# Kernel tuning notes

Measured on AMD Instinct MI355X. Metric: run time of the kernel, lower is better.

Reference implementation:

```python
import jax, jax.numpy as jnp
import numpy as np

B, C, H, W = 16, 256, 32, 32
NUM_LAYERS = 30
OUT = 16  # sqrt(out_channels)
EPS = 1e-5


def setup_inputs() -> dict:
    key = jax.random.key(0)
    k1, k2, k3 = jax.random.split(key, 3)
    x = jax.random.normal(k1, (B, C, H, W), dtype=jnp.float32)
    # delta_t ~ small positive values (module inits ~N(0.01, 0.005))
    delta_t = jax.random.uniform(k2, (NUM_LAYERS, 1), dtype=jnp.float32) * 0.02
    matrices = jax.random.normal(k3, (NUM_LAYERS, 1, 1, OUT, OUT), dtype=jnp.float32) * 0.1
    gamma = jnp.ones((H * W,), dtype=jnp.float32)   # BatchNorm2d weight, oc = i*i = H*W
    beta = jnp.zeros((H * W,), dtype=jnp.float32)   # BatchNorm2d bias
    return {"x": x, "delta_t": delta_t, "matrices": matrices, "gamma": gamma, "beta": beta}


def _bn_relu6(z, gamma, beta):
    # training-mode BatchNorm2d over channel axis 1 (channels = H*W), then ReLU6
    mean = jnp.mean(z, axis=(0, 2, 3), keepdims=True)
    var = jnp.mean(jnp.square(z - mean), axis=(0, 2, 3), keepdims=True)  # biased var
    zhat = (z - mean) * jax.lax.rsqrt(var + EPS)
    g = gamma.reshape(1, -1, 1, 1)
    b = beta.reshape(1, -1, 1, 1)
    return jnp.clip(zhat * g + b, 0.0, 6.0)


def reference(x, delta_t, matrices, gamma, beta):
    b, c, h, w = x.shape
    hw = h * w
    # feature_reshape: [B,C,H,W] -> [B,HW,C] -> [B,HW,out,out] (inn == out branch)
    x1 = x.reshape(b, c, hw).transpose(0, 2, 1).reshape(b, hw, OUT, OUT)
    dt = jnp.clip(delta_t, 0.0, 6.0)[:, 0]  # relu6(delta_t), shape [L]

    def step(y0, params):
        m, dtl = params  # m: [1,1,out,out] broadcasts elementwise against x1
        dydt = -y0 + _bn_relu6(y0 + m * x1, gamma, beta)
        return y0 + dtl * dydt, None

    y0, _ = jax.lax.scan(step, x1, (matrices, dt))
    # (y0 + x1): [B, HW, out, out] -> view [B,H,W,out*out] -> permute to [B,out*out,H,W]
    y = (y0 + x1).reshape(b, h, w, OUT * OUT).transpose(0, 3, 1, 2)
    return y
```

## Files before the change

kernel.cpp:

```cpp
#include <hip/hip_runtime.h>

typedef float v2f __attribute__((ext_vector_type(2)));

#define HW      1024
#define BC      4096
#define NLAYERS 30
#define TPB     256

__global__ __launch_bounds__(TPB) void ode_fused(const float* __restrict__ x,
                                                 const float* __restrict__ delta_t,
                                                 const float* __restrict__ matrices,
                                                 const float* __restrict__ gamma,
                                                 const float* __restrict__ beta,
                                                 float* __restrict__ out) {
    const int bid = blockIdx.x;
    const int p   = ((bid & 7) << 7) | (bid >> 3);
    const int t   = threadIdx.x;

    __shared__ float smat[NLAYERS * 256];
    __shared__ float sdt[NLAYERS];
    __shared__ v2f   red[2][4];

#pragma unroll
    for (int i = 0; i < NLAYERS; ++i)
        smat[i * 256 + t] = matrices[i * 256 + t];
    if (t < NLAYERS)
        sdt[t] = __builtin_amdgcn_fmed3f(delta_t[t], 0.0f, 6.0f);

    v2f x1[8], y[8];
#pragma unroll
    for (int k = 0; k < 8; ++k) {
        x1[k].x = x[(size_t)(t + 512 * k) * HW + p];
        x1[k].y = x[(size_t)(t + 512 * k + 256) * HW + p];
        y[k] = x1[k];
    }

    const float gp   = gamma[p];
    const float bp   = beta[p];
    const int   wid  = t >> 6;
    const int   lane = t & 63;

    __syncthreads();

    for (int l = 0; l < NLAYERS; ++l) {
        const float m   = smat[l * 256 + t];
        const float dtl = sdt[l];
        const v2f m2 = {m, m};

        v2f z[8];
        v2f sA = {0.f, 0.f}, sB = {0.f, 0.f};
        v2f qA = {0.f, 0.f}, qB = {0.f, 0.f};
#pragma unroll
        for (int k = 0; k < 8; k += 2) {
            z[k]     = __builtin_elementwise_fma(m2, x1[k], y[k]);
            z[k + 1] = __builtin_elementwise_fma(m2, x1[k + 1], y[k + 1]);
            sA += z[k];
            sB += z[k + 1];
            qA = __builtin_elementwise_fma(z[k], z[k], qA);
            qB = __builtin_elementwise_fma(z[k + 1], z[k + 1], qB);
        }
        const v2f sv = sA + sB;
        const v2f qv = qA + qB;
        v2f pr; pr.x = sv.x + sv.y; pr.y = qv.x + qv.y;

#pragma unroll
        for (int mask = 1; mask < 64; mask <<= 1) {
            v2f o;
            o.x = __shfl_xor(pr.x, mask, 64);
            o.y = __shfl_xor(pr.y, mask, 64);
            pr += o;
        }
        const int par = l & 1;
        if (lane == 0) red[par][wid] = pr;
        __syncthreads();
        const v2f tot = red[par][0] + red[par][1] + red[par][2] + red[par][3];

        const float mean = tot.x * (1.0f / 4096.0f);
        const float var  = fmaf(-mean, mean, tot.y * (1.0f / 4096.0f));
        const float rstd = rsqrtf(var + 1e-5f);
        const float g    = gp * rstd;
        const float bb   = fmaf(-mean, g, bp);
        const v2f g2  = {g, g},   b2 = {bb, bb};
        const v2f dt2 = {dtl, dtl};
        const v2f z2  = {0.f, 0.f}, s6 = {6.f, 6.f};
#pragma unroll
        for (int k = 0; k < 8; ++k) {
            v2f a = __builtin_elementwise_fma(z[k], g2, b2);
            a = __builtin_elementwise_max(a, z2);
            a = __builtin_elementwise_min(a, s6);
            y[k] = __builtin_elementwise_fma(dt2, a - y[k], y[k]);
        }
    }

#pragma unroll
    for (int k = 0; k < 8; ++k) {
        out[(size_t)(t + 512 * k) * HW + p]       = y[k].x + x1[k].x;
        out[(size_t)(t + 512 * k + 256) * HW + p] = y[k].y + x1[k].y;
    }
}

extern "C" void kernel_launch(void* const* d_in, const int* in_sizes, int n_in,
                              void* d_out, int out_size, void* d_ws, size_t ws_size,
                              hipStream_t stream) {
    const float* x        = (const float*)d_in[0];
    const float* delta_t  = (const float*)d_in[1];
    const float* matrices = (const float*)d_in[2];
    const float* gamma    = (const float*)d_in[3];
    const float* beta     = (const float*)d_in[4];
    float* out = (float*)d_out;

    ode_fused<<<dim3(HW), dim3(TPB), 0, stream>>>(x, delta_t, matrices, gamma, beta, out);
}
```

Measured before the change: 121.7 us.

## Process two BN channels per block with float2 I/O and DPP wave reductions

Each block now handles two adjacent spatial channels with 512 threads instead of one channel with 256, so global loads and stores of x and out become 8-byte float2 accesses. The shuffle-xor reduction is replaced by DPP row/broadcast adds, and the next layer's matrix value and dt are prefetched before the barrier. The update is rewritten as y*(1-dt) + dt*clip(...), with clipping done by fmed3. Halving the grid to 512 blocks may reduce occupancy across CUs.

```diff
diff --git a/kernel.cpp b/kernel.cpp
--- a/kernel.cpp
+++ b/kernel.cpp
@@ -3,9 +3,29 @@
 typedef float v2f __attribute__((ext_vector_type(2)));
 
 #define HW      1024
-#define BC      4096
 #define NLAYERS 30
-#define TPB     256
+#define TPB     512
+
+template <int CTRL, int RMASK>
+__device__ __forceinline__ v2f dpp_add2(v2f x) {
+    int a = __builtin_amdgcn_update_dpp(0, __builtin_bit_cast(int, x.x),
+                                        CTRL, RMASK, 0xf, true);
+    int b = __builtin_amdgcn_update_dpp(0, __builtin_bit_cast(int, x.y),
+                                        CTRL, RMASK, 0xf, true);
+    v2f r;
+    r.x = x.x + __builtin_bit_cast(float, a);
+    r.y = x.y + __builtin_bit_cast(float, b);
+    return r;
+}
+__device__ __forceinline__ v2f wave_sum64_v2(v2f x) {
+    x = dpp_add2<0x111, 0xf>(x);
+    x = dpp_add2<0x112, 0xf>(x);
+    x = dpp_add2<0x114, 0xf>(x);
+    x = dpp_add2<0x118, 0xf>(x);
+    x = dpp_add2<0x142, 0xa>(x);
+    x = dpp_add2<0x143, 0xc>(x);
+    return x;
+}
 
 __global__ __launch_bounds__(TPB) void ode_fused(const float* __restrict__ x,
                                                  const float* __restrict__ delta_t,
@@ -13,39 +33,44 @@
                                                  const float* __restrict__ gamma,
                                                  const float* __restrict__ beta,
                                                  float* __restrict__ out) {
-    const int bid = blockIdx.x;
-    const int p   = ((bid & 7) << 7) | (bid >> 3);
-    const int t   = threadIdx.x;
+    const int bid  = blockIdx.x;
+    const int pA   = ((bid & 7) << 7) | ((bid >> 3) << 1);
+    const int t    = threadIdx.x;
+    const int c    = t & 255;
+    const int wid  = t >> 6;
+    const int lane = t & 63;
 
-    __shared__ float smat[NLAYERS * 256];
-    __shared__ float sdt[NLAYERS];
-    __shared__ v2f   red[2][4];
+    __shared__ float smat[(NLAYERS + 1) * 256];
+    __shared__ float sdt[NLAYERS + 1];
+    __shared__ __align__(16) float4 red[2][8];
 
-#pragma unroll
-    for (int i = 0; i < NLAYERS; ++i)
-        smat[i * 256 + t] = matrices[i * 256 + t];
-    if (t < NLAYERS)
-        sdt[t] = __builtin_amdgcn_fmed3f(delta_t[t], 0.0f, 6.0f);
+    for (int i = t; i < NLAYERS * 256; i += TPB)
+        smat[i] = matrices[i];
+    if (t < NLAYERS) sdt[t] = __builtin_amdgcn_fmed3f(delta_t[t], 0.0f, 6.0f);
+    if (t == 0) sdt[NLAYERS] = 0.0f;
 
+    const float2* __restrict__ xp = (const float2*)(x + pA);
     v2f x1[8], y[8];
 #pragma unroll
     for (int k = 0; k < 8; ++k) {
-        x1[k].x = x[(size_t)(t + 512 * k) * HW + p];
-        x1[k].y = x[(size_t)(t + 512 * k + 256) * HW + p];
+        const float2 v = xp[(size_t)(t + 512 * k) * (HW / 2)];
+        x1[k].x = v.x; x1[k].y = v.y;
         y[k] = x1[k];
     }
 
-    const float gp   = gamma[p];
-    const float bp   = beta[p];
-    const int   wid  = t >> 6;
-    const int   lane = t & 63;
+    const float2 gpv = *(const float2*)(gamma + pA);
+    const float2 bpv = *(const float2*)(beta + pA);
+    const v2f gp2 = {gpv.x, gpv.y};
+    const v2f bp2 = {bpv.x, bpv.y};
 
     __syncthreads();
+    float m_cur = smat[c];
+    float dtl   = sdt[0];
 
     for (int l = 0; l < NLAYERS; ++l) {
-        const float m   = smat[l * 256 + t];
-        const float dtl = sdt[l];
-        const v2f m2 = {m, m};
+        const v2f m2  = {m_cur, m_cur};
+        const v2f dt2 = {dtl, dtl};
+        const v2f om2 = {1.0f - dtl, 1.0f - dtl};
 
         v2f z[8];
         v2f sA = {0.f, 0.f}, sB = {0.f, 0.f};
@@ -59,43 +84,52 @@
             qA = __builtin_elementwise_fma(z[k], z[k], qA);
             qB = __builtin_elementwise_fma(z[k + 1], z[k + 1], qB);
         }
-        const v2f sv = sA + sB;
-        const v2f qv = qA + qB;
-        v2f pr; pr.x = sv.x + sv.y; pr.y = qv.x + qv.y;
+#pragma unroll
+        for (int k = 0; k < 8; ++k) y[k] *= om2;
 
+        const v2f sv = wave_sum64_v2(sA + sB);
+        const v2f qv = wave_sum64_v2(qA + qB);
+
+        const int par = l & 1;
+        if (lane == 63) {
+            float4 w; w.x = sv.x; w.y = sv.y; w.z = qv.x; w.w = qv.y;
+            red[par][wid] = w;
+        }
+        m_cur = smat[(l + 1) * 256 + c];
+        const float dtn = sdt[l + 1];
+        __syncthreads();
+
+        float4 acc = red[par][0];
 #pragma unroll
-        for (int mask = 1; mask < 64; mask <<= 1) {
-            v2f o;
-            o.x = __shfl_xor(pr.x, mask, 64);
-            o.y = __shfl_xor(pr.y, mask, 64);
-            pr += o;
+        for (int w = 1; w < 8; ++w) {
+            const float4 r = red[par][w];
+            acc.x += r.x; acc.y += r.y; acc.z += r.z; acc.w += r.w;
         }
-        const int par = l & 1;
-        if (lane == 0) red[par][wid] = pr;
-        __syncthreads();
-        const v2f tot = red[par][0] + red[par][1] + red[par][2] + red[par][3];
+        const v2f S = {acc.x, acc.y};
+        const v2f Q = {acc.z, acc.w};
 
-        const float mean = tot.x * (1.0f / 4096.0f);
-        const float var  = fmaf(-mean, mean, tot.y * (1.0f / 4096.0f));
-        const float rstd = rsqrtf(var + 1e-5f);
-        const float g    = gp * rstd;
-        const float bb   = fmaf(-mean, g, bp);
-        const v2f g2  = {g, g},   b2 = {bb, bb};
-        const v2f dt2 = {dtl, dtl};
-        const v2f z2  = {0.f, 0.f}, s6 = {6.f, 6.f};
+        const v2f mean = S * (1.0f / 4096.0f);
+        v2f var = Q * (1.0f / 4096.0f) - mean * mean;
+        v2f rstd; rstd.x = rsqrtf(var.x + 1e-5f); rstd.y = rsqrtf(var.y + 1e-5f);
+        const v2f g  = gp2 * rstd;
+        const v2f bb = bp2 - mean * g;
 #pragma unroll
         for (int k = 0; k < 8; ++k) {
-            v2f a = __builtin_elementwise_fma(z[k], g2, b2);
-            a = __builtin_elementwise_max(a, z2);
-            a = __builtin_elementwise_min(a, s6);
-            y[k] = __builtin_elementwise_fma(dt2, a - y[k], y[k]);
+            v2f a = __builtin_elementwise_fma(z[k], g, bb);
+            a.x = __builtin_amdgcn_fmed3f(a.x, 0.0f, 6.0f);
+            a.y = __builtin_amdgcn_fmed3f(a.y, 0.0f, 6.0f);
+            y[k] = __builtin_elementwise_fma(dt2, a, y[k]);
         }
+        dtl = dtn;
     }
 
+    float2* __restrict__ outp = (float2*)(out + pA);
 #pragma unroll
     for (int k = 0; k < 8; ++k) {
-        out[(size_t)(t + 512 * k) * HW + p]       = y[k].x + x1[k].x;
-        out[(size_t)(t + 512 * k + 256) * HW + p] = y[k].y + x1[k].y;
+        float2 w;
+        w.x = y[k].x + x1[k].x;
+        w.y = y[k].y + x1[k].y;
+        outp[(size_t)(t + 512 * k) * (HW / 2)] = w;
     }
 }
 
@@ -109,5 +143,6 @@
     const float* beta     = (const float*)d_in[4];
     float* out = (float*)d_out;
 
-    ode_fused<<<dim3(HW), dim3(TPB), 0, stream>>>(x, delta_t, matrices, gamma, beta, out);
+    ode_fused<<<dim3(HW / 2), dim3(TPB), 0, stream>>>(x, delta_t, matrices,
+                                                      gamma, beta, out);
 }
```

Measured after the change: 123.3 us. No clear change (+1.3%).
